# Performance work log

Measured on AMD Instinct MI355X. Metric: run time of the kernel, lower is better.

## Reference

```python
import jax, jax.numpy as jnp
import numpy as np

B = 65536      # batch (groups of time steps)
T = 5          # time_step
OBS = 128      # unit-data feature dim
ACT = 32       # action feature dim
H = 64         # n_hidden
EPS = 1e-12    # tf.contrib layer_norm epsilon
FORGET_BIAS = 1.0


def _ln_last(x, g, b):
    # layer norm over last axis (2D inputs in the TF graph)
    m = jnp.mean(x, axis=-1, keepdims=True)
    v = jnp.mean(jnp.square(x - m), axis=-1, keepdims=True)
    return (x - m) * jax.lax.rsqrt(v + EPS) * g + b


def _ln_all_but_batch(x, g, b):
    # tf.contrib.layers.layer_norm on 3D input: normalize over axes (1,2), params on last axis
    m = jnp.mean(x, axis=(1, 2), keepdims=True)
    v = jnp.mean(jnp.square(x - m), axis=(1, 2), keepdims=True)
    return (x - m) * jax.lax.rsqrt(v + EPS) * g + b


def _rev_seq(x, au):
    # tf.reverse_sequence along time axis 1 with per-batch lengths au
    t = jnp.arange(T)[None, :]
    idx = jnp.where(t < au[:, None], au[:, None] - 1 - t, t)  # [B, T]
    return jnp.take_along_axis(x, idx[:, :, None], axis=1)


def _lstm(x_btc, au, kernel, bias):
    # BasicLSTMCell (gates i, j, f, o) with sequence_length semantics:
    # past the length, outputs are zero and state is copied through.
    x_tbc = jnp.transpose(x_btc, (1, 0, 2))  # [T, B, C]
    Bn = x_tbc.shape[1]
    c0 = jnp.zeros((Bn, H), x_btc.dtype)
    h0 = jnp.zeros((Bn, H), x_btc.dtype)

    def step(carry, inp):
        c, h = carry
        x_t, t = inp
        valid = (t < au)[:, None]
        gates = jnp.concatenate([x_t, h], axis=-1) @ kernel + bias
        i, j, f, o = jnp.split(gates, 4, axis=-1)
        new_c = jax.nn.sigmoid(f + FORGET_BIAS) * c + jax.nn.sigmoid(i) * jnp.tanh(j)
        new_h = jax.nn.sigmoid(o) * jnp.tanh(new_c)
        c = jnp.where(valid, new_c, c)
        h_carry = jnp.where(valid, new_h, h)
        out = jnp.where(valid, new_h, 0.0)
        return (c, h_carry), out

    (_, _), ys = jax.lax.scan(step, (c0, h0), (x_tbc, jnp.arange(T)))
    return jnp.transpose(ys, (1, 0, 2))  # [B, T, H]


def setup_inputs() -> dict:
    key = jax.random.key(0)
    ks = jax.random.split(key, 12)
    s = 0.05
    return {
        "ud": jax.random.normal(ks[0], (B * T, OBS), jnp.float32),
        "action": jax.random.normal(ks[1], (B * T, ACT), jnp.float32),
        "mask": jax.random.uniform(ks[2], (B, T), jnp.float32),
        "ln0_g": jnp.ones((OBS,), jnp.float32), "ln0_b": jnp.zeros((OBS,), jnp.float32),
        "W1": jax.random.normal(ks[3], (OBS, H), jnp.float32) * s, "b1": jnp.zeros((H,), jnp.float32),
        "ln1_g": jnp.ones((H,), jnp.float32), "ln1_b": jnp.zeros((H,), jnp.float32),
        "W2": jax.random.normal(ks[4], (H + ACT, H), jnp.float32) * s, "b2": jnp.zeros((H,), jnp.float32),
        "ln2_g": jnp.ones((H,), jnp.float32), "ln2_b": jnp.zeros((H,), jnp.float32),
        "fw_k": jax.random.normal(ks[5], (2 * H, 4 * H), jnp.float32) * s,
        "fw_b": jnp.zeros((4 * H,), jnp.float32),
        "bw_k": jax.random.normal(ks[6], (2 * H, 4 * H), jnp.float32) * s,
        "bw_b": jnp.zeros((4 * H,), jnp.float32),
        "ln3_g": jnp.ones((2 * H,), jnp.float32), "ln3_b": jnp.zeros((2 * H,), jnp.float32),
        "conv_w": jax.random.uniform(ks[7], (2 * H,), jnp.float32, -0.003, 0.003),
        "conv_b": jnp.zeros((), jnp.float32),
        "au": jax.random.randint(ks[8], (B,), 1, T + 1, jnp.int32),
    }


def reference(ud, action, mask, ln0_g, ln0_b, W1, b1, ln1_g, ln1_b, W2, b2,
              ln2_g, ln2_b, fw_k, fw_b, bw_k, bw_b, ln3_g, ln3_b,
              conv_w, conv_b, au):
    x = _ln_last(ud, ln0_g, ln0_b)
    x = x @ W1 + b1
    x = jax.nn.relu(_ln_last(x, ln1_g, ln1_b))
    x = jnp.concatenate([x, action], axis=-1)
    x = x @ W2 + b2
    x = jax.nn.relu(_ln_last(x, ln2_g, ln2_b))
    x = x.reshape(B, T, H)
    fw = _lstm(x, au, fw_k, fw_b)
    bw = _rev_seq(_lstm(_rev_seq(x, au), au, bw_k, bw_b), au)
    x = jnp.concatenate([fw, bw], axis=2)                     # [B, T, 2H]
    x = jax.nn.relu(_ln_all_but_batch(x, ln3_g, ln3_b))
    # conv1d with kernel_size=stride=2H on [B, T*2H, 1] == per-step dot product
    q = jnp.einsum('btc,c->bt', x, conv_w) + conv_b           # [B, T]
    Q_mask = q * mask
    Q = jnp.sum(Q_mask, axis=1, keepdims=True)                # [B, 1]
    return Q


if __name__ == "__main__":
    out = reference(**setup_inputs())
    print(out.shape)
```

## Files before the change

kernel.cpp:

```cpp
#include <hip/hip_runtime.h>
#include <hip/hip_bf16.h>

#define NB    65536
#define NT    5
#define NOBS  128
#define NACT  32
#define NH    64

typedef __attribute__((ext_vector_type(8))) short bf16x8;
typedef __attribute__((ext_vector_type(4))) float f32x4;

__device__ __forceinline__ float rcp_fast(float x) { return __builtin_amdgcn_rcpf(x); }
__device__ __forceinline__ float sigf(float x) { return rcp_fast(1.0f + __expf(-x)); }
__device__ __forceinline__ float tanh_fast(float x) { return 1.0f - 2.0f * rcp_fast(__expf(2.0f * x) + 1.0f); }

__device__ __forceinline__ unsigned short f2b(float x) {
  __hip_bfloat16 h = __float2bfloat16(x);
  return *(unsigned short*)&h;
}
__device__ __forceinline__ float b2f(unsigned short u) {
  __hip_bfloat16 h = *(__hip_bfloat16*)&u;
  return __bfloat162float(h);
}
__device__ __forceinline__ void split_bf16(float x, unsigned short& h, unsigned short& l) {
  h = f2b(x);
  l = f2b(x - b2f(h));
}

__global__ __launch_bounds__(256) void k0_prep(
    const float* __restrict__ fk, const float* __restrict__ bk,
    const float* __restrict__ W1, const float* __restrict__ W2,
    const float* __restrict__ ln0g, const float* __restrict__ ln0b,
    const float* __restrict__ b1,
    unsigned int* __restrict__ fkT, unsigned int* __restrict__ bkT,
    unsigned short* __restrict__ w1h, unsigned short* __restrict__ w1l,
    unsigned short* __restrict__ w2h, unsigned short* __restrict__ w2l,
    float* __restrict__ u1, float* __restrict__ vb1) {
  const int bx = blockIdx.x;
  if (bx < 64) {
    const int g  = threadIdx.x;
    const int k0 = bx * 2;
    unsigned int flo = f2b(fk[(k0 + 0) * 256 + g]);
    unsigned int fhi = f2b(fk[(k0 + 1) * 256 + g]);
    unsigned int blo = f2b(bk[(k0 + 0) * 256 + g]);
    unsigned int bhi = f2b(bk[(k0 + 1) * 256 + g]);
    fkT[g * 64 + bx] = flo | (fhi << 16);
    bkT[g * 64 + bx] = blo | (bhi << 16);
    return;
  }
  const int id = (bx - 64) * 256 + threadIdx.x;
  if (id < 1024) {
    const int f = id >> 6, l = id & 63;
    const int kb = f >> 2, nt = f & 3;
    const int q = l >> 4, l16 = l & 15;
    const int n = nt * 16 + l16;
    bf16x8 vh, vl;
#pragma unroll
    for (int j = 0; j < 8; ++j) {
      const int k = kb * 32 + q * 8 + j;
      float wg = ln0g[k] * W1[k * 64 + n];
      unsigned short h, lo;
      split_bf16(wg, h, lo);
      vh[j] = (short)h; vl[j] = (short)lo;
    }
    *(bf16x8*)&w1h[(f * 64 + l) * 8] = vh;
    *(bf16x8*)&w1l[(f * 64 + l) * 8] = vl;
  } else if (id < 1792) {
    const int f = (id - 1024) >> 6, l = id & 63;
    const int kb = f >> 2, nt = f & 3;
    const int q = l >> 4, l16 = l & 15;
    const int n = nt * 16 + l16;
    bf16x8 vh, vl;
#pragma unroll
    for (int j = 0; j < 8; ++j) {
      const int k = kb * 32 + q * 8 + j;
      float wv = W2[k * 64 + n];
      unsigned short h, lo;
      split_bf16(wv, h, lo);
      vh[j] = (short)h; vl[j] = (short)lo;
    }
    *(bf16x8*)&w2h[(f * 64 + l) * 8] = vh;
    *(bf16x8*)&w2l[(f * 64 + l) * 8] = vl;
  } else if (id < 1856) {
    const int n = id - 1792;
    float u = 0.0f, vb = 0.0f;
    for (int k = 0; k < 128; ++k) {
      float wv = W1[k * 64 + n];
      u  += ln0g[k] * wv;
      vb += ln0b[k] * wv;
    }
    u1[n]  = u;
    vb1[n] = vb + b1[n];
  }
}

__global__ __launch_bounds__(256, 4) void k1_mlp(
    const float* __restrict__ ud, const float* __restrict__ action,
    const unsigned short* __restrict__ w1h, const unsigned short* __restrict__ w1l,
    const unsigned short* __restrict__ w2h, const unsigned short* __restrict__ w2l,
    const float* __restrict__ u1, const float* __restrict__ vb1,
    const float* __restrict__ gb2, const float* __restrict__ ln1g,
    const float* __restrict__ ln1b, const float* __restrict__ ln2g,
    const float* __restrict__ ln2b,
    unsigned short* __restrict__ hin) {
  const int wave = threadIdx.x >> 6;
  const int lane = threadIdx.x & 63;
  const int quad = lane >> 4;
  const int l16  = lane & 15;
  const int base = (blockIdx.x * 4 + wave) * 16;

  __shared__ __align__(16) unsigned short lds[4][2][2048];
  unsigned short* x2h = &lds[wave][0][0];
  unsigned short* x2l = &lds[wave][1][0];

  float u1v[4], vbv[4], g1v[4], c1v[4], b2v[4], g2v[4], c2v[4];
#pragma unroll
  for (int nt = 0; nt < 4; ++nt) {
    const int col = nt * 16 + l16;
    u1v[nt] = u1[col];  vbv[nt] = vb1[col];
    g1v[nt] = ln1g[col]; c1v[nt] = ln1b[col];
    b2v[nt] = gb2[col];
    g2v[nt] = ln2g[col]; c2v[nt] = ln2b[col];
  }

  {
    const int arow = lane >> 2, ag = lane & 3;
    const float* ap = &action[(size_t)(base + arow) * NACT + ag * 8];
    float4 a0 = *(const float4*)ap;
    float4 a1 = *(const float4*)(ap + 4);
    float av[8] = {a0.x, a0.y, a0.z, a0.w, a1.x, a1.y, a1.z, a1.w};
    bf16x8 vh, vl;
#pragma unroll
    for (int j = 0; j < 8; ++j) {
      unsigned short h, lo;
      split_bf16(av[j], h, lo);
      vh[j] = (short)h; vl[j] = (short)lo;
    }
    const int idx = arow * 128 + (((8 + ag) ^ (arow & 15)) << 3);
    *(bf16x8*)&x2h[idx] = vh;
    *(bf16x8*)&x2l[idx] = vl;
  }

  const float* rp = &ud[(size_t)(base + l16) * NOBS + quad * 8];
  float4 cfa[4], cfb[4];
#pragma unroll
  for (int kb = 0; kb < 4; ++kb) {
    cfa[kb] = *(const float4*)(rp + kb * 32);
    cfb[kb] = *(const float4*)(rp + kb * 32 + 4);
  }

  bf16x8 W1hf[16], W1lf[16];
#pragma unroll
  for (int f = 0; f < 16; ++f) {
    W1hf[f] = *(const bf16x8*)&w1h[(f * 64 + lane) * 8];
    W1lf[f] = *(const bf16x8*)&w1l[(f * 64 + lane) * 8];
  }

  bf16x8 ones;
#pragma unroll
  for (int j = 0; j < 8; ++j) ones[j] = (short)0x3F80;

  f32x4 acc[4], s_acc, q_acc;
#pragma unroll
  for (int nt = 0; nt < 4; ++nt) acc[nt] = 0.0f;
  s_acc = 0.0f; q_acc = 0.0f;

#pragma unroll
  for (int kb = 0; kb < 4; ++kb) {
    const float xv[8] = {cfa[kb].x, cfa[kb].y, cfa[kb].z, cfa[kb].w,
                         cfb[kb].x, cfb[kb].y, cfb[kb].z, cfb[kb].w};
    bf16x8 Ah, Al, Asq;
#pragma unroll
    for (int j = 0; j < 8; ++j) {
      unsigned short h, lo;
      split_bf16(xv[j], h, lo);
      Ah[j] = (short)h; Al[j] = (short)lo;
      unsigned int uu = ((unsigned int)h) << 16;
      float v = __uint_as_float(uu);
      v *= v;
      Asq[j] = (short)(unsigned short)(__float_as_uint(v) >> 16);
    }
    s_acc = __builtin_amdgcn_mfma_f32_16x16x32_bf16(Ah, ones, s_acc, 0, 0, 0);
    s_acc = __builtin_amdgcn_mfma_f32_16x16x32_bf16(Al, ones, s_acc, 0, 0, 0);
    q_acc = __builtin_amdgcn_mfma_f32_16x16x32_bf16(Asq, ones, q_acc, 0, 0, 0);
#pragma unroll
    for (int nt = 0; nt < 4; ++nt) {
      const int f = kb * 4 + nt;
      acc[nt] = __builtin_amdgcn_mfma_f32_16x16x32_bf16(Ah, W1hf[f], acc[nt], 0, 0, 0);
      acc[nt] = __builtin_amdgcn_mfma_f32_16x16x32_bf16(Ah, W1lf[f], acc[nt], 0, 0, 0);
      acc[nt] = __builtin_amdgcn_mfma_f32_16x16x32_bf16(Al, W1hf[f], acc[nt], 0, 0, 0);
    }
  }

  float inv0[4], ivm[4];
#pragma unroll
  for (int r = 0; r < 4; ++r) {
    float m   = s_acc[r] * (1.0f / 128.0f);
    float var = q_acc[r] * (1.0f / 128.0f) - m * m;
    float inv = rsqrtf(var + 1e-12f);
    inv0[r] = inv;
    ivm[r]  = inv * m;
  }
  float y[4][4];
#pragma unroll
  for (int nt = 0; nt < 4; ++nt)
#pragma unroll
    for (int r = 0; r < 4; ++r)
      y[nt][r] = fmaf(inv0[r], acc[nt][r], fmaf(-ivm[r], u1v[nt], vbv[nt]));

  float m1[4], i1[4];
#pragma unroll
  for (int r = 0; r < 4; ++r) {
    float s1 = y[0][r] + y[1][r] + y[2][r] + y[3][r];
    float q1 = y[0][r] * y[0][r] + y[1][r] * y[1][r] +
               y[2][r] * y[2][r] + y[3][r] * y[3][r];
#pragma unroll
    for (int off = 1; off <= 8; off <<= 1) {
      s1 += __shfl_xor(s1, off, 64);
      q1 += __shfl_xor(q1, off, 64);
    }
    float mm = s1 * (1.0f / 64.0f);
    m1[r] = mm;
    i1[r] = rsqrtf(q1 * (1.0f / 64.0f) - mm * mm + 1e-12f);
  }

#pragma unroll
  for (int nt = 0; nt < 4; ++nt)
#pragma unroll
    for (int r = 0; r < 4; ++r) {
      float x1 = fmaxf(0.0f, fmaf((y[nt][r] - m1[r]) * i1[r], g1v[nt], c1v[nt]));
      unsigned short h, lo;
      split_bf16(x1, h, lo);
      const int row = quad * 4 + r;
      const int idx = row * 128 + (((nt * 2 + (l16 >> 3)) ^ (row & 15)) << 3) + (l16 & 7);
      x2h[idx] = h;
      x2l[idx] = lo;
    }

  f32x4 acc2[4];
#pragma unroll
  for (int nt = 0; nt < 4; ++nt) acc2[nt] = 0.0f;

#pragma unroll
  for (int kb = 0; kb < 3; ++kb) {
    bf16x8 w2hf[4], w2lf[4];
#pragma unroll
    for (int nt = 0; nt < 4; ++nt) {
      const int f = kb * 4 + nt;
      w2hf[nt] = *(const bf16x8*)&w2h[(f * 64 + lane) * 8];
      w2lf[nt] = *(const bf16x8*)&w2l[(f * 64 + lane) * 8];
    }
    const int ai = l16 * 128 + (((kb * 4 + quad) ^ l16) << 3);
    bf16x8 Ah = *(const bf16x8*)&x2h[ai];
    bf16x8 Al = *(const bf16x8*)&x2l[ai];
#pragma unroll
    for (int nt = 0; nt < 4; ++nt) {
      acc2[nt] = __builtin_amdgcn_mfma_f32_16x16x32_bf16(Ah, w2hf[nt], acc2[nt], 0, 0, 0);
      acc2[nt] = __builtin_amdgcn_mfma_f32_16x16x32_bf16(Ah, w2lf[nt], acc2[nt], 0, 0, 0);
      acc2[nt] = __builtin_amdgcn_mfma_f32_16x16x32_bf16(Al, w2hf[nt], acc2[nt], 0, 0, 0);
    }
  }

  float y2[4][4];
#pragma unroll
  for (int nt = 0; nt < 4; ++nt)
#pragma unroll
    for (int r = 0; r < 4; ++r)
      y2[nt][r] = acc2[nt][r] + b2v[nt];

  float m2[4], i2[4];
#pragma unroll
  for (int r = 0; r < 4; ++r) {
    float s2 = y2[0][r] + y2[1][r] + y2[2][r] + y2[3][r];
    float q2 = y2[0][r] * y2[0][r] + y2[1][r] * y2[1][r] +
               y2[2][r] * y2[2][r] + y2[3][r] * y2[3][r];
#pragma unroll
    for (int off = 1; off <= 8; off <<= 1) {
      s2 += __shfl_xor(s2, off, 64);
      q2 += __shfl_xor(q2, off, 64);
    }
    float mm = s2 * (1.0f / 64.0f);
    m2[r] = mm;
    i2[r] = rsqrtf(q2 * (1.0f / 64.0f) - mm * mm + 1e-12f);
  }

#pragma unroll
  for (int nt = 0; nt < 4; ++nt)
#pragma unroll
    for (int r = 0; r < 4; ++r) {
      float o = fmaxf(0.0f, fmaf((y2[nt][r] - m2[r]) * i2[r], g2v[nt], c2v[nt]));
      const int row = quad * 4 + r;
      hin[(size_t)(base + row) * NH + nt * 16 + l16] = f2b(o);
    }
}

__global__ __launch_bounds__(256, 2) void k23_lstm_final(
    const unsigned short* __restrict__ hin,
    const unsigned short* __restrict__ fkT, const float* __restrict__ fwb,
    const unsigned short* __restrict__ bkT, const float* __restrict__ bwb,
    const int* __restrict__ au,
    const float* __restrict__ ln3g, const float* __restrict__ ln3b,
    const float* __restrict__ conv_w, const float* __restrict__ conv_b,
    const float* __restrict__ mask, float* __restrict__ out) {
  const int tid  = threadIdx.x;
  const int w    = tid >> 6;
  const int lane = tid & 63;
  const int quad = lane >> 4;
  const int l16  = lane & 15;
  const int batch0 = blockIdx.x * 32;

  __shared__ __align__(16) unsigned short obuf[10 * 32 * 64];
  __shared__ __align__(16) unsigned short hA[2][32 * 64];

  const int u = w * 16 + l16;

  const int aum0 = au[batch0 + l16];
  const int aum1 = au[batch0 + 16 + l16];
  int aur[8];
#pragma unroll
  for (int mt = 0; mt < 2; ++mt)
#pragma unroll
    for (int r = 0; r < 4; ++r)
      aur[mt * 4 + r] = au[batch0 + mt * 16 + quad * 4 + r];

  for (int dir = 0; dir < 2; ++dir) {
    const unsigned short* kT   = dir ? bkT : fkT;
    const float*          bias = dir ? bwb : fwb;

    bf16x8 Bf[4][4];
#pragma unroll
    for (int g = 0; g < 4; ++g) {
      const int n = g * 64 + u;
#pragma unroll
      for (int kb = 0; kb < 4; ++kb)
        Bf[g][kb] = *(const bf16x8*)&kT[n * 128 + kb * 32 + quad * 8];
    }
    const float bg0 = bias[u], bg1 = bias[64 + u];
    const float bg2 = bias[128 + u] + 1.0f, bg3 = bias[192 + u];

    *(float4*)&hA[0][tid * 8] = make_float4(0.f, 0.f, 0.f, 0.f);
    float c_s[8], h_s[8];
#pragma unroll
    for (int i = 0; i < 8; ++i) { c_s[i] = 0.0f; h_s[i] = 0.0f; }
    __syncthreads();

    bf16x8 Ax0[2], Ax1[2];
#pragma unroll
    for (int mt = 0; mt < 2; ++mt) {
      const int m = mt * 16 + l16;
      const int a = mt ? aum1 : aum0;
      const int st = dir ? (a - 1) : 0;
      const size_t rb = ((size_t)(batch0 + m) * NT + st) * NH;
      Ax0[mt] = *(const bf16x8*)&hin[rb + quad * 8];
      Ax1[mt] = *(const bf16x8*)&hin[rb + 32 + quad * 8];
    }

    int cur = 0;
    for (int t = 0; t < NT; ++t) {
      const int nxt = cur ^ 1;
      f32x4 acc[2][4];
#pragma unroll
      for (int mt = 0; mt < 2; ++mt) {
        acc[mt][0] = bg0; acc[mt][1] = bg1; acc[mt][2] = bg2; acc[mt][3] = bg3;
      }

#pragma unroll
      for (int mt = 0; mt < 2; ++mt) {
        const int m = mt * 16 + l16;
        bf16x8 Ah0 = *(const bf16x8*)&hA[cur][m * 64 + ((quad ^ (m & 7)) << 3)];
        bf16x8 Ah1 = *(const bf16x8*)&hA[cur][m * 64 + (((4 + quad) ^ (m & 7)) << 3)];
#pragma unroll
        for (int g = 0; g < 4; ++g) {
          acc[mt][g] = __builtin_amdgcn_mfma_f32_16x16x32_bf16(Ax0[mt], Bf[g][0], acc[mt][g], 0, 0, 0);
          acc[mt][g] = __builtin_amdgcn_mfma_f32_16x16x32_bf16(Ax1[mt], Bf[g][1], acc[mt][g], 0, 0, 0);
          acc[mt][g] = __builtin_amdgcn_mfma_f32_16x16x32_bf16(Ah0, Bf[g][2], acc[mt][g], 0, 0, 0);
          acc[mt][g] = __builtin_amdgcn_mfma_f32_16x16x32_bf16(Ah1, Bf[g][3], acc[mt][g], 0, 0, 0);
        }
      }

      if (t < NT - 1) {
        const int t2 = t + 1;
#pragma unroll
        for (int mt = 0; mt < 2; ++mt) {
          const int m = mt * 16 + l16;
          const int a = mt ? aum1 : aum0;
          const int st = dir ? ((t2 < a) ? (a - 1 - t2) : t2) : t2;
          const size_t rb = ((size_t)(batch0 + m) * NT + st) * NH;
          Ax0[mt] = *(const bf16x8*)&hin[rb + quad * 8];
          Ax1[mt] = *(const bf16x8*)&hin[rb + 32 + quad * 8];
        }
      }

#pragma unroll
      for (int mt = 0; mt < 2; ++mt) {
#pragma unroll
        for (int r = 0; r < 4; ++r) {
          const int idx = mt * 4 + r;
          const int bl = mt * 16 + quad * 4 + r;
          const int a  = aur[idx];
          float gi = acc[mt][0][r];
          float gj = acc[mt][1][r];
          float gf = acc[mt][2][r];
          float go = acc[mt][3][r];
          float nc = sigf(gf) * c_s[idx] + sigf(gi) * tanh_fast(gj);
          float nh = sigf(go) * tanh_fast(nc);
          bool valid = t < a;
          c_s[idx] = valid ? nc : c_s[idx];
          h_s[idx] = valid ? nh : h_s[idx];
          float outv = valid ? nh : 0.0f;
          int pos = dir ? (valid ? (a - 1 - t) : t) : t;
          unsigned int pk;
          asm("v_cvt_pk_bf16_f32 %0, %1, %2" : "=v"(pk) : "v"(outv), "v"(h_s[idx]));
          obuf[(dir * 5 + pos) * 2048 + bl * 64 + u] = (unsigned short)pk;
          hA[nxt][bl * 64 + (((u >> 3) ^ (bl & 7)) << 3) + (u & 7)] =
              (unsigned short)(pk >> 16);
        }
      }
      __syncthreads();
      cur = nxt;
    }
  }

  const float gl  = ln3g[lane],      gh  = ln3g[64 + lane];
  const float bl3 = ln3b[lane],      bh3 = ln3b[64 + lane];
  const float cwl = conv_w[lane],    cwh = conv_w[64 + lane];
  const float cb  = conv_b[0];

  for (int bb = w * 8; bb < w * 8 + 8; bb += 2) {
    float v0[2][NT], v1[2][NT];
#pragma unroll
    for (int u2 = 0; u2 < 2; ++u2)
#pragma unroll
      for (int p = 0; p < NT; ++p) {
        v0[u2][p] = b2f(obuf[p * 2048 + (bb + u2) * 64 + lane]);
        v1[u2][p] = b2f(obuf[(5 + p) * 2048 + (bb + u2) * 64 + lane]);
      }
    float s[2], q[2];
#pragma unroll
    for (int u2 = 0; u2 < 2; ++u2) {
      s[u2] = 0.0f; q[u2] = 0.0f;
#pragma unroll
      for (int p = 0; p < NT; ++p) {
        s[u2] += v0[u2][p] + v1[u2][p];
        q[u2] += v0[u2][p] * v0[u2][p] + v1[u2][p] * v1[u2][p];
      }
    }
#pragma unroll
    for (int off = 32; off; off >>= 1) {
      s[0] += __shfl_xor(s[0], off, 64);
      q[0] += __shfl_xor(q[0], off, 64);
      s[1] += __shfl_xor(s[1], off, 64);
      q[1] += __shfl_xor(q[1], off, 64);
    }
    float local[2], msum[2];
#pragma unroll
    for (int u2 = 0; u2 < 2; ++u2) {
      const int b = batch0 + bb + u2;
      float m   = s[u2] * (1.0f / 640.0f);
      float var = q[u2] * (1.0f / 640.0f) - m * m;
      float inv = __builtin_amdgcn_rsqf(var + 1e-12f);
      float acc = 0.0f, ms = 0.0f;
#pragma unroll
      for (int p = 0; p < NT; ++p) {
        float mk = mask[b * NT + p];
        ms += mk;
        float xf = fmaxf(0.0f, (v0[u2][p] - m) * inv * gl + bl3);
        float xb = fmaxf(0.0f, (v1[u2][p] - m) * inv * gh + bh3);
        acc += mk * (xf * cwl + xb * cwh);
      }
      local[u2] = acc; msum[u2] = ms;
    }
#pragma unroll
    for (int off = 32; off; off >>= 1) {
      local[0] += __shfl_xor(local[0], off, 64);
      local[1] += __shfl_xor(local[1], off, 64);
    }
    if (lane == 0) {
      out[batch0 + bb]     = local[0] + cb * msum[0];
      out[batch0 + bb + 1] = local[1] + cb * msum[1];
    }
  }
}

extern "C" void kernel_launch(void* const* d_in, const int* in_sizes, int n_in,
                              void* d_out, int out_size, void* d_ws, size_t ws_size,
                              hipStream_t stream) {
  const float* ud     = (const float*)d_in[0];
  const float* action = (const float*)d_in[1];
  const float* mask   = (const float*)d_in[2];
  const float* ln0g   = (const float*)d_in[3];
  const float* ln0b   = (const float*)d_in[4];
  const float* W1     = (const float*)d_in[5];
  const float* b1     = (const float*)d_in[6];
  const float* ln1g   = (const float*)d_in[7];
  const float* ln1b   = (const float*)d_in[8];
  const float* W2     = (const float*)d_in[9];
  const float* b2     = (const float*)d_in[10];
  const float* ln2g   = (const float*)d_in[11];
  const float* ln2b   = (const float*)d_in[12];
  const float* fwk    = (const float*)d_in[13];
  const float* fwb    = (const float*)d_in[14];
  const float* bwk    = (const float*)d_in[15];
  const float* bwb    = (const float*)d_in[16];
  const float* ln3g   = (const float*)d_in[17];
  const float* ln3b   = (const float*)d_in[18];
  const float* conv_w = (const float*)d_in[19];
  const float* conv_b = (const float*)d_in[20];
  const int*   au     = (const int*)d_in[21];

  const size_t n_hin = (size_t)NB * NT * NH;
  unsigned short* wsu   = (unsigned short*)d_ws;
  unsigned short* hin   = wsu;
  unsigned short* fkT   = hin + n_hin;
  unsigned short* bkT   = fkT + 32768;
  unsigned short* w1h   = bkT + 32768;
  unsigned short* w1l   = w1h + 8192;
  unsigned short* w2h   = w1l + 8192;
  unsigned short* w2l   = w2h + 6144;
  float*          u1    = (float*)(w2l + 6144);
  float*          vb1   = u1 + 64;

  float* outf = (float*)d_out;

  k0_prep<<<72, 256, 0, stream>>>(fwk, bwk, W1, W2, ln0g, ln0b, b1,
                                  (unsigned int*)fkT, (unsigned int*)bkT,
                                  w1h, w1l, w2h, w2l, u1, vb1);
  k1_mlp<<<(NB * NT) / 64, 256, 0, stream>>>(ud, action, w1h, w1l, w2h, w2l,
                                             u1, vb1, b2, ln1g, ln1b, ln2g, ln2b,
                                             hin);
  k23_lstm_final<<<NB / 32, 256, 0, stream>>>(hin, fkT, fwb, bkT, bwb, au,
                                              ln3g, ln3b, conv_w, conv_b,
                                              mask, outf);
}
```

Measured before the change: 452.8 us.

## Fuse MLP and bidirectional LSTM kernels, keeping hidden inputs in LDS

Merges the MLP kernel into the LSTM/final kernel. Each block now computes the MLP for its 16 batches (80 rows) and writes the bf16 activations to shared memory instead of a global hin buffer, then runs both LSTM directions from LDS. This removes the global write and read of the intermediate tensor and one kernel launch. In exchange, each block processes 16 instead of 32 batches, so LSTM MFMA work per step halves and there are more __syncthreads per unit of work. The MLP phase uses only 5 tiles over 4 waves, which leaves waves idle, and the launch bound is lowered to 3 blocks per CU.

```diff
diff --git a/kernel.cpp b/kernel.cpp
--- a/kernel.cpp
+++ b/kernel.cpp
@@ -94,7 +94,7 @@
   }
 }
 
-__global__ __launch_bounds__(256, 4) void k1_mlp(
+__global__ __launch_bounds__(256, 3) void k123_fused(
     const float* __restrict__ ud, const float* __restrict__ action,
     const unsigned short* __restrict__ w1h, const unsigned short* __restrict__ w1l,
     const unsigned short* __restrict__ w2h, const unsigned short* __restrict__ w2l,
@@ -102,200 +102,6 @@
     const float* __restrict__ gb2, const float* __restrict__ ln1g,
     const float* __restrict__ ln1b, const float* __restrict__ ln2g,
     const float* __restrict__ ln2b,
-    unsigned short* __restrict__ hin) {
-  const int wave = threadIdx.x >> 6;
-  const int lane = threadIdx.x & 63;
-  const int quad = lane >> 4;
-  const int l16  = lane & 15;
-  const int base = (blockIdx.x * 4 + wave) * 16;
-
-  __shared__ __align__(16) unsigned short lds[4][2][2048];
-  unsigned short* x2h = &lds[wave][0][0];
-  unsigned short* x2l = &lds[wave][1][0];
-
-  float u1v[4], vbv[4], g1v[4], c1v[4], b2v[4], g2v[4], c2v[4];
-#pragma unroll
-  for (int nt = 0; nt < 4; ++nt) {
-    const int col = nt * 16 + l16;
-    u1v[nt] = u1[col];  vbv[nt] = vb1[col];
-    g1v[nt] = ln1g[col]; c1v[nt] = ln1b[col];
-    b2v[nt] = gb2[col];
-    g2v[nt] = ln2g[col]; c2v[nt] = ln2b[col];
-  }
-
-  {
-    const int arow = lane >> 2, ag = lane & 3;
-    const float* ap = &action[(size_t)(base + arow) * NACT + ag * 8];
-    float4 a0 = *(const float4*)ap;
-    float4 a1 = *(const float4*)(ap + 4);
-    float av[8] = {a0.x, a0.y, a0.z, a0.w, a1.x, a1.y, a1.z, a1.w};
-    bf16x8 vh, vl;
-#pragma unroll
-    for (int j = 0; j < 8; ++j) {
-      unsigned short h, lo;
-      split_bf16(av[j], h, lo);
-      vh[j] = (short)h; vl[j] = (short)lo;
-    }
-    const int idx = arow * 128 + (((8 + ag) ^ (arow & 15)) << 3);
-    *(bf16x8*)&x2h[idx] = vh;
-    *(bf16x8*)&x2l[idx] = vl;
-  }
-
-  const float* rp = &ud[(size_t)(base + l16) * NOBS + quad * 8];
-  float4 cfa[4], cfb[4];
-#pragma unroll
-  for (int kb = 0; kb < 4; ++kb) {
-    cfa[kb] = *(const float4*)(rp + kb * 32);
-    cfb[kb] = *(const float4*)(rp + kb * 32 + 4);
-  }
-
-  bf16x8 W1hf[16], W1lf[16];
-#pragma unroll
-  for (int f = 0; f < 16; ++f) {
-    W1hf[f] = *(const bf16x8*)&w1h[(f * 64 + lane) * 8];
-    W1lf[f] = *(const bf16x8*)&w1l[(f * 64 + lane) * 8];
-  }
-
-  bf16x8 ones;
-#pragma unroll
-  for (int j = 0; j < 8; ++j) ones[j] = (short)0x3F80;
-
-  f32x4 acc[4], s_acc, q_acc;
-#pragma unroll
-  for (int nt = 0; nt < 4; ++nt) acc[nt] = 0.0f;
-  s_acc = 0.0f; q_acc = 0.0f;
-
-#pragma unroll
-  for (int kb = 0; kb < 4; ++kb) {
-    const float xv[8] = {cfa[kb].x, cfa[kb].y, cfa[kb].z, cfa[kb].w,
-                         cfb[kb].x, cfb[kb].y, cfb[kb].z, cfb[kb].w};
-    bf16x8 Ah, Al, Asq;
-#pragma unroll
-    for (int j = 0; j < 8; ++j) {
-      unsigned short h, lo;
-      split_bf16(xv[j], h, lo);
-      Ah[j] = (short)h; Al[j] = (short)lo;
-      unsigned int uu = ((unsigned int)h) << 16;
-      float v = __uint_as_float(uu);
-      v *= v;
-      Asq[j] = (short)(unsigned short)(__float_as_uint(v) >> 16);
-    }
-    s_acc = __builtin_amdgcn_mfma_f32_16x16x32_bf16(Ah, ones, s_acc, 0, 0, 0);
-    s_acc = __builtin_amdgcn_mfma_f32_16x16x32_bf16(Al, ones, s_acc, 0, 0, 0);
-    q_acc = __builtin_amdgcn_mfma_f32_16x16x32_bf16(Asq, ones, q_acc, 0, 0, 0);
-#pragma unroll
-    for (int nt = 0; nt < 4; ++nt) {
-      const int f = kb * 4 + nt;
-      acc[nt] = __builtin_amdgcn_mfma_f32_16x16x32_bf16(Ah, W1hf[f], acc[nt], 0, 0, 0);
-      acc[nt] = __builtin_amdgcn_mfma_f32_16x16x32_bf16(Ah, W1lf[f], acc[nt], 0, 0, 0);
-      acc[nt] = __builtin_amdgcn_mfma_f32_16x16x32_bf16(Al, W1hf[f], acc[nt], 0, 0, 0);
-    }
-  }
-
-  float inv0[4], ivm[4];
-#pragma unroll
-  for (int r = 0; r < 4; ++r) {
-    float m   = s_acc[r] * (1.0f / 128.0f);
-    float var = q_acc[r] * (1.0f / 128.0f) - m * m;
-    float inv = rsqrtf(var + 1e-12f);
-    inv0[r] = inv;
-    ivm[r]  = inv * m;
-  }
-  float y[4][4];
-#pragma unroll
-  for (int nt = 0; nt < 4; ++nt)
-#pragma unroll
-    for (int r = 0; r < 4; ++r)
-      y[nt][r] = fmaf(inv0[r], acc[nt][r], fmaf(-ivm[r], u1v[nt], vbv[nt]));
-
-  float m1[4], i1[4];
-#pragma unroll
-  for (int r = 0; r < 4; ++r) {
-    float s1 = y[0][r] + y[1][r] + y[2][r] + y[3][r];
-    float q1 = y[0][r] * y[0][r] + y[1][r] * y[1][r] +
-               y[2][r] * y[2][r] + y[3][r] * y[3][r];
-#pragma unroll
-    for (int off = 1; off <= 8; off <<= 1) {
-      s1 += __shfl_xor(s1, off, 64);
-      q1 += __shfl_xor(q1, off, 64);
-    }
-    float mm = s1 * (1.0f / 64.0f);
-    m1[r] = mm;
-    i1[r] = rsqrtf(q1 * (1.0f / 64.0f) - mm * mm + 1e-12f);
-  }
-
-#pragma unroll
-  for (int nt = 0; nt < 4; ++nt)
-#pragma unroll
-    for (int r = 0; r < 4; ++r) {
-      float x1 = fmaxf(0.0f, fmaf((y[nt][r] - m1[r]) * i1[r], g1v[nt], c1v[nt]));
-      unsigned short h, lo;
-      split_bf16(x1, h, lo);
-      const int row = quad * 4 + r;
-      const int idx = row * 128 + (((nt * 2 + (l16 >> 3)) ^ (row & 15)) << 3) + (l16 & 7);
-      x2h[idx] = h;
-      x2l[idx] = lo;
-    }
-
-  f32x4 acc2[4];
-#pragma unroll
-  for (int nt = 0; nt < 4; ++nt) acc2[nt] = 0.0f;
-
-#pragma unroll
-  for (int kb = 0; kb < 3; ++kb) {
-    bf16x8 w2hf[4], w2lf[4];
-#pragma unroll
-    for (int nt = 0; nt < 4; ++nt) {
-      const int f = kb * 4 + nt;
-      w2hf[nt] = *(const bf16x8*)&w2h[(f * 64 + lane) * 8];
-      w2lf[nt] = *(const bf16x8*)&w2l[(f * 64 + lane) * 8];
-    }
-    const int ai = l16 * 128 + (((kb * 4 + quad) ^ l16) << 3);
-    bf16x8 Ah = *(const bf16x8*)&x2h[ai];
-    bf16x8 Al = *(const bf16x8*)&x2l[ai];
-#pragma unroll
-    for (int nt = 0; nt < 4; ++nt) {
-      acc2[nt] = __builtin_amdgcn_mfma_f32_16x16x32_bf16(Ah, w2hf[nt], acc2[nt], 0, 0, 0);
-      acc2[nt] = __builtin_amdgcn_mfma_f32_16x16x32_bf16(Ah, w2lf[nt], acc2[nt], 0, 0, 0);
-      acc2[nt] = __builtin_amdgcn_mfma_f32_16x16x32_bf16(Al, w2hf[nt], acc2[nt], 0, 0, 0);
-    }
-  }
-
-  float y2[4][4];
-#pragma unroll
-  for (int nt = 0; nt < 4; ++nt)
-#pragma unroll
-    for (int r = 0; r < 4; ++r)
-      y2[nt][r] = acc2[nt][r] + b2v[nt];
-
-  float m2[4], i2[4];
-#pragma unroll
-  for (int r = 0; r < 4; ++r) {
-    float s2 = y2[0][r] + y2[1][r] + y2[2][r] + y2[3][r];
-    float q2 = y2[0][r] * y2[0][r] + y2[1][r] * y2[1][r] +
-               y2[2][r] * y2[2][r] + y2[3][r] * y2[3][r];
-#pragma unroll
-    for (int off = 1; off <= 8; off <<= 1) {
-      s2 += __shfl_xor(s2, off, 64);
-      q2 += __shfl_xor(q2, off, 64);
-    }
-    float mm = s2 * (1.0f / 64.0f);
-    m2[r] = mm;
-    i2[r] = rsqrtf(q2 * (1.0f / 64.0f) - mm * mm + 1e-12f);
-  }
-
-#pragma unroll
-  for (int nt = 0; nt < 4; ++nt)
-#pragma unroll
-    for (int r = 0; r < 4; ++r) {
-      float o = fmaxf(0.0f, fmaf((y2[nt][r] - m2[r]) * i2[r], g2v[nt], c2v[nt]));
-      const int row = quad * 4 + r;
-      hin[(size_t)(base + row) * NH + nt * 16 + l16] = f2b(o);
-    }
-}
-
-__global__ __launch_bounds__(256, 2) void k23_lstm_final(
-    const unsigned short* __restrict__ hin,
     const unsigned short* __restrict__ fkT, const float* __restrict__ fwb,
     const unsigned short* __restrict__ bkT, const float* __restrict__ bwb,
     const int* __restrict__ au,
@@ -307,21 +113,216 @@
   const int lane = tid & 63;
   const int quad = lane >> 4;
   const int l16  = lane & 15;
-  const int batch0 = blockIdx.x * 32;
-
-  __shared__ __align__(16) unsigned short obuf[10 * 32 * 64];
-  __shared__ __align__(16) unsigned short hA[2][32 * 64];
+  const int batch0 = blockIdx.x * 16;
+
+  __shared__ __align__(16) unsigned short smem[16384];
+  unsigned short* mlp   = smem;
+  unsigned short* obufS = smem + 5120;
+  unsigned short* hA    = smem + 15360;
+
+  {
+    float u1v[4], vbv[4], g1v[4], c1v[4], b2v[4], g2v[4], c2v[4];
+#pragma unroll
+    for (int nt = 0; nt < 4; ++nt) {
+      const int col = nt * 16 + l16;
+      u1v[nt] = u1[col];  vbv[nt] = vb1[col];
+      g1v[nt] = ln1g[col]; c1v[nt] = ln1b[col];
+      b2v[nt] = gb2[col];
+      g2v[nt] = ln2g[col]; c2v[nt] = ln2b[col];
+    }
+    unsigned short* x2h = obufS + w * 2048;
+    unsigned short* x2l = x2h + 1024;
+
+    bf16x8 ones;
+#pragma unroll
+    for (int j = 0; j < 8; ++j) ones[j] = (short)0x3F80;
+
+    for (int tile = w; tile < 5; tile += 4) {
+      const int rbase = blockIdx.x * 80 + tile * 16;
+
+      const float* rp = &ud[(size_t)(rbase + l16) * NOBS + quad * 8];
+      float4 cfa[4], cfb[4];
+#pragma unroll
+      for (int kb = 0; kb < 4; ++kb) {
+        cfa[kb] = *(const float4*)(rp + kb * 32);
+        cfb[kb] = *(const float4*)(rp + kb * 32 + 4);
+      }
+
+      f32x4 acc[4], s_acc, q_acc;
+#pragma unroll
+      for (int nt = 0; nt < 4; ++nt) acc[nt] = 0.0f;
+      s_acc = 0.0f; q_acc = 0.0f;
+
+#pragma unroll
+      for (int kb = 0; kb < 4; ++kb) {
+        bf16x8 W1hfk[4], W1lfk[4];
+#pragma unroll
+        for (int nt = 0; nt < 4; ++nt) {
+          const int f = kb * 4 + nt;
+          W1hfk[nt] = *(const bf16x8*)&w1h[(f * 64 + lane) * 8];
+          W1lfk[nt] = *(const bf16x8*)&w1l[(f * 64 + lane) * 8];
+        }
+        const float xv[8] = {cfa[kb].x, cfa[kb].y, cfa[kb].z, cfa[kb].w,
+                             cfb[kb].x, cfb[kb].y, cfb[kb].z, cfb[kb].w};
+        bf16x8 Ah, Al, Asq;
+#pragma unroll
+        for (int j = 0; j < 8; ++j) {
+          unsigned short h, lo;
+          split_bf16(xv[j], h, lo);
+          Ah[j] = (short)h; Al[j] = (short)lo;
+          unsigned int uu = ((unsigned int)h) << 16;
+          float v = __uint_as_float(uu);
+          v *= v;
+          Asq[j] = (short)(unsigned short)(__float_as_uint(v) >> 16);
+        }
+        s_acc = __builtin_amdgcn_mfma_f32_16x16x32_bf16(Ah, ones, s_acc, 0, 0, 0);
+        s_acc = __builtin_amdgcn_mfma_f32_16x16x32_bf16(Al, ones, s_acc, 0, 0, 0);
+        q_acc = __builtin_amdgcn_mfma_f32_16x16x32_bf16(Asq, ones, q_acc, 0, 0, 0);
+#pragma unroll
+        for (int nt = 0; nt < 4; ++nt) {
+          acc[nt] = __builtin_amdgcn_mfma_f32_16x16x32_bf16(Ah, W1hfk[nt], acc[nt], 0, 0, 0);
+          acc[nt] = __builtin_amdgcn_mfma_f32_16x16x32_bf16(Ah, W1lfk[nt], acc[nt], 0, 0, 0);
+          acc[nt] = __builtin_amdgcn_mfma_f32_16x16x32_bf16(Al, W1hfk[nt], acc[nt], 0, 0, 0);
+        }
+      }
+
+      float inv0[4], ivm[4];
+#pragma unroll
+      for (int r = 0; r < 4; ++r) {
+        float m   = s_acc[r] * (1.0f / 128.0f);
+        float var = q_acc[r] * (1.0f / 128.0f) - m * m;
+        float inv = rsqrtf(var + 1e-12f);
+        inv0[r] = inv;
+        ivm[r]  = inv * m;
+      }
+      float y[4][4];
+#pragma unroll
+      for (int nt = 0; nt < 4; ++nt)
+#pragma unroll
+        for (int r = 0; r < 4; ++r)
+          y[nt][r] = fmaf(inv0[r], acc[nt][r], fmaf(-ivm[r], u1v[nt], vbv[nt]));
+
+      float m1[4], i1[4];
+#pragma unroll
+      for (int r = 0; r < 4; ++r) {
+        float s1 = y[0][r] + y[1][r] + y[2][r] + y[3][r];
+        float q1 = y[0][r] * y[0][r] + y[1][r] * y[1][r] +
+                   y[2][r] * y[2][r] + y[3][r] * y[3][r];
+#pragma unroll
+        for (int off = 1; off <= 8; off <<= 1) {
+          s1 += __shfl_xor(s1, off, 64);
+          q1 += __shfl_xor(q1, off, 64);
+        }
+        float mm = s1 * (1.0f / 64.0f);
+        m1[r] = mm;
+        i1[r] = rsqrtf(q1 * (1.0f / 64.0f) - mm * mm + 1e-12f);
+      }
+
+#pragma unroll
+      for (int nt = 0; nt < 4; ++nt)
+#pragma unroll
+        for (int r = 0; r < 4; ++r) {
+          float x1 = fmaxf(0.0f, fmaf((y[nt][r] - m1[r]) * i1[r], g1v[nt], c1v[nt]));
+          unsigned short h, lo;
+          split_bf16(x1, h, lo);
+          const int row = quad * 4 + r;
+          const int idx = row * 64 + (((nt * 2 + (l16 >> 3)) ^ (row & 7)) << 3) + (l16 & 7);
+          x2h[idx] = h;
+          x2l[idx] = lo;
+        }
+
+      f32x4 acc2[4];
+#pragma unroll
+      for (int nt = 0; nt < 4; ++nt) acc2[nt] = 0.0f;
+
+#pragma unroll
+      for (int kb = 0; kb < 2; ++kb) {
+        bf16x8 w2hf[4], w2lf[4];
+#pragma unroll
+        for (int nt = 0; nt < 4; ++nt) {
+          const int f = kb * 4 + nt;
+          w2hf[nt] = *(const bf16x8*)&w2h[(f * 64 + lane) * 8];
+          w2lf[nt] = *(const bf16x8*)&w2l[(f * 64 + lane) * 8];
+        }
+        const int ai = l16 * 64 + (((kb * 4 + quad) ^ (l16 & 7)) << 3);
+        bf16x8 Ah = *(const bf16x8*)&x2h[ai];
+        bf16x8 Al = *(const bf16x8*)&x2l[ai];
+#pragma unroll
+        for (int nt = 0; nt < 4; ++nt) {
+          acc2[nt] = __builtin_amdgcn_mfma_f32_16x16x32_bf16(Ah, w2hf[nt], acc2[nt], 0, 0, 0);
+          acc2[nt] = __builtin_amdgcn_mfma_f32_16x16x32_bf16(Ah, w2lf[nt], acc2[nt], 0, 0, 0);
+          acc2[nt] = __builtin_amdgcn_mfma_f32_16x16x32_bf16(Al, w2hf[nt], acc2[nt], 0, 0, 0);
+        }
+      }
+
+      {
+        const float* apg = &action[(size_t)(rbase + l16) * NACT + quad * 8];
+        float4 a0 = *(const float4*)apg;
+        float4 a1 = *(const float4*)(apg + 4);
+        const float av[8] = {a0.x, a0.y, a0.z, a0.w, a1.x, a1.y, a1.z, a1.w};
+        bf16x8 Ah, Al;
+#pragma unroll
+        for (int j = 0; j < 8; ++j) {
+          unsigned short h, lo;
+          split_bf16(av[j], h, lo);
+          Ah[j] = (short)h; Al[j] = (short)lo;
+        }
+        bf16x8 w2hf[4], w2lf[4];
+#pragma unroll
+        for (int nt = 0; nt < 4; ++nt) {
+          const int f = 8 + nt;
+          w2hf[nt] = *(const bf16x8*)&w2h[(f * 64 + lane) * 8];
+          w2lf[nt] = *(const bf16x8*)&w2l[(f * 64 + lane) * 8];
+        }
+#pragma unroll
+        for (int nt = 0; nt < 4; ++nt) {
+          acc2[nt] = __builtin_amdgcn_mfma_f32_16x16x32_bf16(Ah, w2hf[nt], acc2[nt], 0, 0, 0);
+          acc2[nt] = __builtin_amdgcn_mfma_f32_16x16x32_bf16(Ah, w2lf[nt], acc2[nt], 0, 0, 0);
+          acc2[nt] = __builtin_amdgcn_mfma_f32_16x16x32_bf16(Al, w2hf[nt], acc2[nt], 0, 0, 0);
+        }
+      }
+
+      float y2[4][4];
+#pragma unroll
+      for (int nt = 0; nt < 4; ++nt)
+#pragma unroll
+        for (int r = 0; r < 4; ++r)
+          y2[nt][r] = acc2[nt][r] + b2v[nt];
+
+      float m2[4], i2[4];
+#pragma unroll
+      for (int r = 0; r < 4; ++r) {
+        float s2 = y2[0][r] + y2[1][r] + y2[2][r] + y2[3][r];
+        float q2 = y2[0][r] * y2[0][r] + y2[1][r] * y2[1][r] +
+                   y2[2][r] * y2[2][r] + y2[3][r] * y2[3][r];
+#pragma unroll
+        for (int off = 1; off <= 8; off <<= 1) {
+          s2 += __shfl_xor(s2, off, 64);
+          q2 += __shfl_xor(q2, off, 64);
+        }
+        float mm = s2 * (1.0f / 64.0f);
+        m2[r] = mm;
+        i2[r] = rsqrtf(q2 * (1.0f / 64.0f) - mm * mm + 1e-12f);
+      }
+
+#pragma unroll
+      for (int nt = 0; nt < 4; ++nt)
+#pragma unroll
+        for (int r = 0; r < 4; ++r) {
+          float o = fmaxf(0.0f, fmaf((y2[nt][r] - m2[r]) * i2[r], g2v[nt], c2v[nt]));
+          const int lr = tile * 16 + quad * 4 + r;
+          const int idx = lr * 64 + (((nt * 2 + (l16 >> 3)) ^ (lr & 7)) << 3) + (l16 & 7);
+          mlp[idx] = f2b(o);
+        }
+    }
+  }
+  __syncthreads();
 
   const int u = w * 16 + l16;
-
   const int aum0 = au[batch0 + l16];
-  const int aum1 = au[batch0 + 16 + l16];
-  int aur[8];
-#pragma unroll
-  for (int mt = 0; mt < 2; ++mt)
-#pragma unroll
-    for (int r = 0; r < 4; ++r)
-      aur[mt * 4 + r] = au[batch0 + mt * 16 + quad * 4 + r];
+  int aur[4];
+#pragma unroll
+  for (int r = 0; r < 4; ++r) aur[r] = au[batch0 + quad * 4 + r];
 
   for (int dir = 0; dir < 2; ++dir) {
     const unsigned short* kT   = dir ? bkT : fkT;
@@ -338,86 +339,57 @@
     const float bg0 = bias[u], bg1 = bias[64 + u];
     const float bg2 = bias[128 + u] + 1.0f, bg3 = bias[192 + u];
 
-    *(float4*)&hA[0][tid * 8] = make_float4(0.f, 0.f, 0.f, 0.f);
-    float c_s[8], h_s[8];
-#pragma unroll
-    for (int i = 0; i < 8; ++i) { c_s[i] = 0.0f; h_s[i] = 0.0f; }
+    *(float2*)&hA[tid * 4] = make_float2(0.f, 0.f);
+    float c_s[4], h_s[4];
+#pragma unroll
+    for (int i = 0; i < 4; ++i) { c_s[i] = 0.0f; h_s[i] = 0.0f; }
     __syncthreads();
 
-    bf16x8 Ax0[2], Ax1[2];
-#pragma unroll
-    for (int mt = 0; mt < 2; ++mt) {
-      const int m = mt * 16 + l16;
-      const int a = mt ? aum1 : aum0;
-      const int st = dir ? (a - 1) : 0;
-      const size_t rb = ((size_t)(batch0 + m) * NT + st) * NH;
-      Ax0[mt] = *(const bf16x8*)&hin[rb + quad * 8];
-      Ax1[mt] = *(const bf16x8*)&hin[rb + 32 + quad * 8];
-    }
-
-    int cur = 0;
     for (int t = 0; t < NT; ++t) {
-      const int nxt = cur ^ 1;
-      f32x4 acc[2][4];
-#pragma unroll
-      for (int mt = 0; mt < 2; ++mt) {
-        acc[mt][0] = bg0; acc[mt][1] = bg1; acc[mt][2] = bg2; acc[mt][3] = bg3;
-      }
-
-#pragma unroll
-      for (int mt = 0; mt < 2; ++mt) {
-        const int m = mt * 16 + l16;
-        bf16x8 Ah0 = *(const bf16x8*)&hA[cur][m * 64 + ((quad ^ (m & 7)) << 3)];
-        bf16x8 Ah1 = *(const bf16x8*)&hA[cur][m * 64 + (((4 + quad) ^ (m & 7)) << 3)];
-#pragma unroll
-        for (int g = 0; g < 4; ++g) {
-          acc[mt][g] = __builtin_amdgcn_mfma_f32_16x16x32_bf16(Ax0[mt], Bf[g][0], acc[mt][g], 0, 0, 0);
-          acc[mt][g] = __builtin_amdgcn_mfma_f32_16x16x32_bf16(Ax1[mt], Bf[g][1], acc[mt][g], 0, 0, 0);
-          acc[mt][g] = __builtin_amdgcn_mfma_f32_16x16x32_bf16(Ah0, Bf[g][2], acc[mt][g], 0, 0, 0);
-          acc[mt][g] = __builtin_amdgcn_mfma_f32_16x16x32_bf16(Ah1, Bf[g][3], acc[mt][g], 0, 0, 0);
-        }
-      }
-
-      if (t < NT - 1) {
-        const int t2 = t + 1;
-#pragma unroll
-        for (int mt = 0; mt < 2; ++mt) {
-          const int m = mt * 16 + l16;
-          const int a = mt ? aum1 : aum0;
-          const int st = dir ? ((t2 < a) ? (a - 1 - t2) : t2) : t2;
-          const size_t rb = ((size_t)(batch0 + m) * NT + st) * NH;
-          Ax0[mt] = *(const bf16x8*)&hin[rb + quad * 8];
-          Ax1[mt] = *(const bf16x8*)&hin[rb + 32 + quad * 8];
-        }
-      }
-
-#pragma unroll
-      for (int mt = 0; mt < 2; ++mt) {
-#pragma unroll
-        for (int r = 0; r < 4; ++r) {
-          const int idx = mt * 4 + r;
-          const int bl = mt * 16 + quad * 4 + r;
-          const int a  = aur[idx];
-          float gi = acc[mt][0][r];
-          float gj = acc[mt][1][r];
-          float gf = acc[mt][2][r];
-          float go = acc[mt][3][r];
-          float nc = sigf(gf) * c_s[idx] + sigf(gi) * tanh_fast(gj);
-          float nh = sigf(go) * tanh_fast(nc);
-          bool valid = t < a;
-          c_s[idx] = valid ? nc : c_s[idx];
-          h_s[idx] = valid ? nh : h_s[idx];
-          float outv = valid ? nh : 0.0f;
-          int pos = dir ? (valid ? (a - 1 - t) : t) : t;
-          unsigned int pk;
-          asm("v_cvt_pk_bf16_f32 %0, %1, %2" : "=v"(pk) : "v"(outv), "v"(h_s[idx]));
-          obuf[(dir * 5 + pos) * 2048 + bl * 64 + u] = (unsigned short)pk;
-          hA[nxt][bl * 64 + (((u >> 3) ^ (bl & 7)) << 3) + (u & 7)] =
-              (unsigned short)(pk >> 16);
-        }
+      f32x4 acc[4];
+      acc[0] = bg0; acc[1] = bg1; acc[2] = bg2; acc[3] = bg3;
+
+      const int a0t = aum0;
+      const int st  = dir ? ((t < a0t) ? (a0t - 1 - t) : t) : t;
+      const int row = l16 * 5 + st;
+      const int s7  = row & 7;
+      bf16x8 Ax0 = *(const bf16x8*)&mlp[row * 64 + ((quad ^ s7) << 3)];
+      bf16x8 Ax1 = *(const bf16x8*)&mlp[row * 64 + (((4 + quad) ^ s7) << 3)];
+      const int h7 = l16 & 7;
+      bf16x8 Ah0 = *(const bf16x8*)&hA[l16 * 64 + ((quad ^ h7) << 3)];
+      bf16x8 Ah1 = *(const bf16x8*)&hA[l16 * 64 + (((4 + quad) ^ h7) << 3)];
+
+#pragma unroll
+      for (int g = 0; g < 4; ++g) {
+        acc[g] = __builtin_amdgcn_mfma_f32_16x16x32_bf16(Ax0, Bf[g][0], acc[g], 0, 0, 0);
+        acc[g] = __builtin_amdgcn_mfma_f32_16x16x32_bf16(Ax1, Bf[g][1], acc[g], 0, 0, 0);
+        acc[g] = __builtin_amdgcn_mfma_f32_16x16x32_bf16(Ah0, Bf[g][2], acc[g], 0, 0, 0);
+        acc[g] = __builtin_amdgcn_mfma_f32_16x16x32_bf16(Ah1, Bf[g][3], acc[g], 0, 0, 0);
       }
       __syncthreads();
-      cur = nxt;
+
+#pragma unroll
+      for (int r = 0; r < 4; ++r) {
+        const int bl = quad * 4 + r;
+        const int a  = aur[r];
+        float gi = acc[0][r];
+        float gj = acc[1][r];
+        float gf = acc[2][r];
+        float go = acc[3][r];
+        float nc = sigf(gf) * c_s[r] + sigf(gi) * tanh_fast(gj);
+        float nh = sigf(go) * tanh_fast(nc);
+        bool valid = t < a;
+        c_s[r] = valid ? nc : c_s[r];
+        h_s[r] = valid ? nh : h_s[r];
+        float outv = valid ? nh : 0.0f;
+        int pos = dir ? (valid ? (a - 1 - t) : t) : t;
+        unsigned int pk;
+        asm("v_cvt_pk_bf16_f32 %0, %1, %2" : "=v"(pk) : "v"(outv), "v"(h_s[r]));
+        obufS[(dir * 5 + pos) * 1024 + bl * 64 + u] = (unsigned short)pk;
+        hA[bl * 64 + (((u >> 3) ^ (bl & 7)) << 3) + (u & 7)] =
+            (unsigned short)(pk >> 16);
+      }
+      __syncthreads();
     }
   }
 
@@ -426,14 +398,14 @@
   const float cwl = conv_w[lane],    cwh = conv_w[64 + lane];
   const float cb  = conv_b[0];
 
-  for (int bb = w * 8; bb < w * 8 + 8; bb += 2) {
+  for (int bb = w * 4; bb < w * 4 + 4; bb += 2) {
     float v0[2][NT], v1[2][NT];
 #pragma unroll
     for (int u2 = 0; u2 < 2; ++u2)
 #pragma unroll
       for (int p = 0; p < NT; ++p) {
-        v0[u2][p] = b2f(obuf[p * 2048 + (bb + u2) * 64 + lane]);
-        v1[u2][p] = b2f(obuf[(5 + p) * 2048 + (bb + u2) * 64 + lane]);
+        v0[u2][p] = b2f(obufS[p * 1024 + (bb + u2) * 64 + lane]);
+        v1[u2][p] = b2f(obufS[(5 + p) * 1024 + (bb + u2) * 64 + lane]);
       }
     float s[2], q[2];
 #pragma unroll
@@ -508,10 +480,8 @@
   const float* conv_b = (const float*)d_in[20];
   const int*   au     = (const int*)d_in[21];
 
-  const size_t n_hin = (size_t)NB * NT * NH;
   unsigned short* wsu   = (unsigned short*)d_ws;
-  unsigned short* hin   = wsu;
-  unsigned short* fkT   = hin + n_hin;
+  unsigned short* fkT   = wsu;
   unsigned short* bkT   = fkT + 32768;
   unsigned short* w1h   = bkT + 32768;
   unsigned short* w1l   = w1h + 8192;
@@ -525,10 +495,9 @@
   k0_prep<<<72, 256, 0, stream>>>(fwk, bwk, W1, W2, ln0g, ln0b, b1,
                                   (unsigned int*)fkT, (unsigned int*)bkT,
                                   w1h, w1l, w2h, w2l, u1, vb1);
-  k1_mlp<<<(NB * NT) / 64, 256, 0, stream>>>(ud, action, w1h, w1l, w2h, w2l,
-                                             u1, vb1, b2, ln1g, ln1b, ln2g, ln2b,
-                                             hin);
-  k23_lstm_final<<<NB / 32, 256, 0, stream>>>(hin, fkT, fwb, bkT, bwb, au,
-                                              ln3g, ln3b, conv_w, conv_b,
-                                              mask, outf);
+  k123_fused<<<NB / 16, 256, 0, stream>>>(ud, action, w1h, w1l, w2h, w2l,
+                                          u1, vb1, b2, ln1g, ln1b, ln2g, ln2b,
+                                          fkT, fwb, bkT, bwb, au,
+                                          ln3g, ln3b, conv_w, conv_b,
+                                          mask, outf);
 }
```

New measurement: 777.6 us. +71.7%, slower.
